# Kernel optimization log

Hardware: AMD Instinct MI355X
Metric: run time of the kernel (lower is better)

## Reference

```python
import jax, jax.numpy as jnp
import numpy as np

B, H, S, DK = 4, 12, 2048, 64

def setup_inputs() -> dict:
    key = jax.random.key(0)
    kq, kk, kv = jax.random.split(key, 3)
    Q = jax.random.normal(kq, (B, H, S, DK), dtype=jnp.float32)
    K = jax.random.normal(kk, (B, H, S, DK), dtype=jnp.float32)
    V = jax.random.normal(kv, (B, H, S, DK), dtype=jnp.float32)
    return {"Q": Q, "K": K, "V": V, "d_k": DK}

def reference(Q, K, V, d_k):
    scale = 1.0 / jnp.sqrt(jnp.float32(d_k))
    # scores: [B, H, S, S]
    scores = jnp.einsum('bhqd,bhkd->bhqk', Q, K) * scale
    attn = jax.nn.softmax(scores, axis=-1)
    context = jnp.einsum('bhqk,bhkd->bhqd', attn, V)
    return (context, attn)
```

## Files before the change

### kernel.cpp

```cpp
#include <hip/hip_runtime.h>


#define S_LEN 2048
#define D_K   64
#define NBH   48
#define VT_STRIDE 2080
#define CH    128
#define NCHUNK (S_LEN / CH)

typedef __attribute__((ext_vector_type(8))) short short8v;
typedef __attribute__((ext_vector_type(4))) short short4v;
typedef __attribute__((ext_vector_type(4))) float float4v;

__device__ inline unsigned short f2bf(float f) {
    union { float f; unsigned u; } c; c.f = f;
    unsigned u = c.u;
    return (unsigned short)((u + 0x7FFFu + ((u >> 16) & 1u)) >> 16);
}
__device__ inline float bf2f(unsigned short h) {
    union { unsigned u; float f; } c; c.u = ((unsigned)h) << 16; return c.f;
}

__device__ inline void wg_sync_lds() {
    asm volatile("s_waitcnt lgkmcnt(0)" ::: "memory");
    __builtin_amdgcn_s_barrier();
    __builtin_amdgcn_sched_barrier(0);
}

#define CEXP 0.18033688011112042f

__global__ __launch_bounds__(256)
void conv_k_kernel(const float* __restrict__ K, unsigned short* __restrict__ Kbf) {
    const size_t N = (size_t)NBH * S_LEN * D_K;
    for (size_t i = ((size_t)blockIdx.x * 256 + threadIdx.x) * 4; i < N;
         i += (size_t)gridDim.x * 256 * 4) {
        float4v v = *reinterpret_cast<const float4v*>(K + i);
        unsigned p0 = (unsigned)f2bf(v[0]) | ((unsigned)f2bf(v[1]) << 16);
        unsigned p1 = (unsigned)f2bf(v[2]) | ((unsigned)f2bf(v[3]) << 16);
        uint2 pk; pk.x = p0; pk.y = p1;
        *reinterpret_cast<uint2*>(Kbf + i) = pk;
    }
}

__global__ __launch_bounds__(256)
void trans_v_kernel(const float* __restrict__ V, unsigned short* __restrict__ VT) {
    const int bh = blockIdx.y;
    const int k0 = blockIdx.x * 64;
    __shared__ unsigned short tile[64][66];
    const int t = threadIdx.x;
    {
        const int kr = t >> 2, dq = t & 3;
        const float* src = V + (size_t)bh * S_LEN * D_K + (size_t)(k0 + kr) * D_K + dq * 16;
        #pragma unroll
        for (int i = 0; i < 4; ++i) {
            float4v v = *reinterpret_cast<const float4v*>(src + i * 4);
            #pragma unroll
            for (int j = 0; j < 4; ++j) tile[kr][dq * 16 + i * 4 + j] = f2bf(v[j]);
        }
    }
    __syncthreads();
    {
        const int d = t >> 2, kq = t & 3;
        unsigned pk[8];
        #pragma unroll
        for (int i = 0; i < 8; ++i) {
            unsigned lo = tile[kq * 16 + 2 * i][d];
            unsigned hi = tile[kq * 16 + 2 * i + 1][d];
            pk[i] = lo | (hi << 16);
        }
        unsigned* dst = reinterpret_cast<unsigned*>(
            VT + (size_t)bh * D_K * VT_STRIDE + (size_t)d * VT_STRIDE + k0 + kq * 16);
        uint4 a; a.x = pk[0]; a.y = pk[1]; a.z = pk[2]; a.w = pk[3];
        uint4 b; b.x = pk[4]; b.y = pk[5]; b.z = pk[6]; b.w = pk[7];
        reinterpret_cast<uint4*>(dst)[0] = a;
        reinterpret_cast<uint4*>(dst)[1] = b;
    }
}

__global__ __launch_bounds__(512, 6)
void sdpa_fused_kernel(const float* __restrict__ Qp,
                       const unsigned short* __restrict__ Kbf,
                       const unsigned short* __restrict__ VT,
                       float* __restrict__ ctx, float* __restrict__ attn) {
    const int qt   = blockIdx.x;
    const int bh   = blockIdx.y;
    const int tid  = threadIdx.x;
    const int w    = tid >> 6;
    const int lane = tid & 63;
    const int lq   = lane & 15;
    const int lg   = lane >> 4;
    const int qg   = qt * 128 + w * 16;
    const size_t base = (size_t)bh * S_LEN * D_K;

    __shared__ __align__(16) unsigned short kbuf[128 * 64];
    __shared__ __align__(16) unsigned short vbuf[64 * 128];
    __shared__ __align__(16) unsigned short pbw[8][16][40];

    short8v q0, q1;
    {
        const float* qr = Qp + base + (size_t)(qg + lq) * D_K + lg * 8;
        float4v qa = *reinterpret_cast<const float4v*>(qr);
        float4v qb = *reinterpret_cast<const float4v*>(qr + 4);
        float4v qc = *reinterpret_cast<const float4v*>(qr + 32);
        float4v qd = *reinterpret_cast<const float4v*>(qr + 36);
        #pragma unroll
        for (int j = 0; j < 4; ++j) {
            q0[j]     = (short)f2bf(qa[j]);
            q0[4 + j] = (short)f2bf(qb[j]);
            q1[j]     = (short)f2bf(qc[j]);
            q1[4 + j] = (short)f2bf(qd[j]);
        }
    }

    const int krow  = tid >> 2;
    const int kby0  = (tid & 3) * 16;
    const int kbi0  = krow * 64 + (((kby0)      ^ ((krow & 7) << 4)) >> 1);
    const int kbi1  = krow * 64 + (((kby0 + 64) ^ ((krow & 7) << 4)) >> 1);
    const unsigned short* ksrcb = Kbf + base + (size_t)krow * D_K + (kby0 >> 1);

    const int vrow  = tid >> 3;
    const int vby0  = (tid & 7) * 16;
    const int vbi0  = vrow * 128 + (((vby0)       ^ ((vrow & 15) << 4)) >> 1);
    const int vbi1  = vrow * 128 + (((vby0 + 128) ^ ((vrow & 15) << 4)) >> 1);
    const unsigned short* vsrcb = VT + (size_t)bh * D_K * VT_STRIDE
                                     + (size_t)vrow * VT_STRIDE + (vby0 >> 1);

    const int kswz = (lq & 7) << 4;
    const int koff0 = ((lg * 16)      ^ kswz) >> 1;
    const int koff1 = ((64 + lg * 16) ^ kswz) >> 1;
    const int vswz = lq << 4;

    float s = 0.f;
    for (int c = 0; c < NCHUNK; ++c) {
        short8v kr0 = *reinterpret_cast<const short8v*>(ksrcb + (size_t)c * CH * D_K);
        short8v kr1 = *reinterpret_cast<const short8v*>(ksrcb + (size_t)c * CH * D_K + 32);
        wg_sync_lds();
        *reinterpret_cast<short8v*>(&kbuf[kbi0]) = kr0;
        *reinterpret_cast<short8v*>(&kbuf[kbi1]) = kr1;
        wg_sync_lds();
        #pragma unroll
        for (int kt = 0; kt < 8; ++kt) {
            const int kl = kt * 16 + lq;
            short8v k0 = *reinterpret_cast<const short8v*>(&kbuf[kl * 64 + koff0]);
            short8v k1 = *reinterpret_cast<const short8v*>(&kbuf[kl * 64 + koff1]);
            float4v a = (float4v)0.0f;
            a = __builtin_amdgcn_mfma_f32_16x16x32_bf16(k0, q0, a, 0, 0, 0);
            a = __builtin_amdgcn_mfma_f32_16x16x32_bf16(k1, q1, a, 0, 0, 0);
            s += exp2f(a[0] * CEXP) + exp2f(a[1] * CEXP)
               + exp2f(a[2] * CEXP) + exp2f(a[3] * CEXP);
        }
    }
    s += __shfl_xor(s, 16, 64);
    s += __shfl_xor(s, 32, 64);
    const float rs_a = 1.0f / s;

    float4v cacc[4];
    #pragma unroll
    for (int dt = 0; dt < 4; ++dt) cacc[dt] = (float4v)0.0f;

    float* attnb = attn + (size_t)bh * S_LEN * S_LEN;

    for (int c = 0; c < NCHUNK; ++c) {
        short8v kr0 = *reinterpret_cast<const short8v*>(ksrcb + (size_t)c * CH * D_K);
        short8v kr1 = *reinterpret_cast<const short8v*>(ksrcb + (size_t)c * CH * D_K + 32);
        short8v vr0 = *reinterpret_cast<const short8v*>(vsrcb + c * CH);
        short8v vr1 = *reinterpret_cast<const short8v*>(vsrcb + c * CH + 64);
        wg_sync_lds();
        *reinterpret_cast<short8v*>(&kbuf[kbi0]) = kr0;
        *reinterpret_cast<short8v*>(&kbuf[kbi1]) = kr1;
        *reinterpret_cast<short8v*>(&vbuf[vbi0]) = vr0;
        *reinterpret_cast<short8v*>(&vbuf[vbi1]) = vr1;
        wg_sync_lds();

        #pragma unroll
        for (int s2 = 0; s2 < 4; ++s2) {
            #pragma unroll
            for (int t = 0; t < 2; ++t) {
                const int kt = s2 * 2 + t;
                const int kl = kt * 16 + lq;
                short8v k0 = *reinterpret_cast<const short8v*>(&kbuf[kl * 64 + koff0]);
                short8v k1 = *reinterpret_cast<const short8v*>(&kbuf[kl * 64 + koff1]);
                float4v a = (float4v)0.0f;
                a = __builtin_amdgcn_mfma_f32_16x16x32_bf16(k0, q0, a, 0, 0, 0);
                a = __builtin_amdgcn_mfma_f32_16x16x32_bf16(k1, q1, a, 0, 0, 0);
                float p0 = exp2f(a[0] * CEXP) * rs_a;
                float p1 = exp2f(a[1] * CEXP) * rs_a;
                float p2 = exp2f(a[2] * CEXP) * rs_a;
                float p3 = exp2f(a[3] * CEXP) * rs_a;
                uint2 pkv;
                pkv.x = (unsigned)f2bf(p0) | ((unsigned)f2bf(p1) << 16);
                pkv.y = (unsigned)f2bf(p2) | ((unsigned)f2bf(p3) << 16);
                *reinterpret_cast<uint2*>(&pbw[w][lq][t * 16 + lg * 4]) = pkv;
            }
            #pragma unroll
            for (int r2 = 0; r2 < 2; ++r2) {
                const int row = r2 * 8 + (lane >> 3);
                short4v p4 = *reinterpret_cast<const short4v*>(&pbw[w][row][(lane & 7) * 4]);
                float4v o;
                o[0] = bf2f((unsigned short)p4[0]);
                o[1] = bf2f((unsigned short)p4[1]);
                o[2] = bf2f((unsigned short)p4[2]);
                o[3] = bf2f((unsigned short)p4[3]);
                *reinterpret_cast<float4v*>(
                    &attnb[(size_t)(qg + row) * S_LEN + c * CH + s2 * 32 + (lane & 7) * 4]) = o;
            }
            short8v pa = *reinterpret_cast<const short8v*>(&pbw[w][lq][lg * 8]);
            #pragma unroll
            for (int dt = 0; dt < 4; ++dt) {
                const int d = dt * 16 + lq;
                short8v bv = *reinterpret_cast<const short8v*>(
                    &vbuf[d * 128 + (((s2 * 64 + lg * 16) ^ vswz) >> 1)]);
                cacc[dt] = __builtin_amdgcn_mfma_f32_16x16x32_bf16(pa, bv, cacc[dt], 0, 0, 0);
            }
        }
    }

    float* ctxb = ctx + base;
    #pragma unroll
    for (int dt = 0; dt < 4; ++dt)
        #pragma unroll
        for (int r = 0; r < 4; ++r)
            ctxb[(size_t)(qg + lg * 4 + r) * D_K + dt * 16 + lq] = cacc[dt][r];
}

__global__ __launch_bounds__(512)
void sdpa_fallback_kernel(const float* __restrict__ Qp, const float* __restrict__ Kp,
                          const float* __restrict__ Vp,
                          float* __restrict__ ctx, float* __restrict__ attn) {
    const int qt = blockIdx.x, bh = blockIdx.y, tid = threadIdx.x;
    const int w = tid >> 6, lane = tid & 63, lq = lane & 15, lg = lane >> 4;
    const int qg = qt * 16, kw = w * 256;
    const size_t base = (size_t)bh * S_LEN * D_K;
    __shared__ __align__(16) char smem_raw[8 * 16 * 136 * 2];
    __shared__ float red_s[16][8];
    auto pbuf = reinterpret_cast<unsigned short(*)[16][136]>(smem_raw);
    auto ctxp = reinterpret_cast<float(*)[16][64]>(smem_raw);

    short8v q0, q1;
    {
        const float* qr = Qp + base + (size_t)(qg + lq) * D_K + lg * 8;
        #pragma unroll
        for (int j = 0; j < 8; ++j) { q0[j] = (short)f2bf(qr[j]); q1[j] = (short)f2bf(qr[32 + j]); }
    }
    float4v acc[16];
    #pragma unroll
    for (int kt = 0; kt < 16; ++kt) acc[kt] = (float4v)0.0f;
    #pragma unroll
    for (int kt = 0; kt < 16; ++kt) {
        const float* kr = Kp + base + (size_t)(kw + kt * 16 + lq) * D_K + lg * 8;
        short8v k0, k1;
        #pragma unroll
        for (int j = 0; j < 8; ++j) { k0[j] = (short)f2bf(kr[j]); k1[j] = (short)f2bf(kr[32 + j]); }
        acc[kt] = __builtin_amdgcn_mfma_f32_16x16x32_bf16(k0, q0, acc[kt], 0, 0, 0);
        acc[kt] = __builtin_amdgcn_mfma_f32_16x16x32_bf16(k1, q1, acc[kt], 0, 0, 0);
    }
    float s = 0.f;
    #pragma unroll
    for (int kt = 0; kt < 16; ++kt)
        #pragma unroll
        for (int r = 0; r < 4; ++r) {
            float p = exp2f(acc[kt][r] * CEXP);
            acc[kt][r] = p; s += p;
        }
    s += __shfl_xor(s, 16, 64);
    s += __shfl_xor(s, 32, 64);
    if (lane < 16) red_s[lane][w] = s;
    __syncthreads();
    float gs = red_s[lq][0];
    #pragma unroll
    for (int ww = 1; ww < 8; ++ww) gs += red_s[lq][ww];
    const float rsv = 1.0f / gs;
    #pragma unroll
    for (int kt = 0; kt < 16; ++kt) acc[kt] = acc[kt] * rsv;

    float4v cacc[4];
    #pragma unroll
    for (int dt = 0; dt < 4; ++dt) cacc[dt] = (float4v)0.0f;
    #pragma unroll
    for (int half = 0; half < 2; ++half) {
        #pragma unroll
        for (int kth = 0; kth < 8; ++kth) {
            const int kt = half * 8 + kth;
            unsigned p01 = (unsigned)f2bf(acc[kt][0]) | ((unsigned)f2bf(acc[kt][1]) << 16);
            unsigned p23 = (unsigned)f2bf(acc[kt][2]) | ((unsigned)f2bf(acc[kt][3]) << 16);
            unsigned* dst = reinterpret_cast<unsigned*>(&pbuf[w][lq][kth * 16 + lg * 4]);
            dst[0] = p01; dst[1] = p23;
        }
        #pragma unroll
        for (int s2 = 0; s2 < 4; ++s2) {
            short8v pa = *reinterpret_cast<const short8v*>(&pbuf[w][lq][s2 * 32 + lg * 8]);
            const int kk = kw + half * 128 + s2 * 32 + lg * 8;
            #pragma unroll
            for (int dt = 0; dt < 4; ++dt) {
                short8v bv;
                #pragma unroll
                for (int j = 0; j < 8; ++j)
                    bv[j] = (short)f2bf(Vp[base + (size_t)(kk + j) * D_K + dt * 16 + lq]);
                cacc[dt] = __builtin_amdgcn_mfma_f32_16x16x32_bf16(pa, bv, cacc[dt], 0, 0, 0);
            }
        }
    }
    __syncthreads();
    #pragma unroll
    for (int dt = 0; dt < 4; ++dt)
        #pragma unroll
        for (int r = 0; r < 4; ++r)
            ctxp[w][lg * 4 + r][dt * 16 + lq] = cacc[dt][r];
    __syncthreads();
    float* ctxb = ctx + base;
    for (int idx = tid; idx < 16 * 64; idx += 512) {
        const int q = idx >> 6, d = idx & 63;
        float sum = 0.f;
        #pragma unroll
        for (int ww = 0; ww < 8; ++ww) sum += ctxp[ww][q][d];
        ctxb[(size_t)(qg + q) * D_K + d] = sum;
    }
    float* attnb = attn + (size_t)bh * S_LEN * S_LEN + (size_t)(qg + lq) * S_LEN + kw + lg * 4;
    #pragma unroll
    for (int kt = 0; kt < 16; ++kt)
        *reinterpret_cast<float4v*>(attnb + kt * 16) = acc[kt];
}

extern "C" void kernel_launch(void* const* d_in, const int* in_sizes, int n_in,
                              void* d_out, int out_size, void* d_ws, size_t ws_size,
                              hipStream_t stream) {
    const float* Q = (const float*)d_in[0];
    const float* K = (const float*)d_in[1];
    const float* V = (const float*)d_in[2];
    float* ctx  = (float*)d_out;
    float* attn = ctx + (size_t)NBH * S_LEN * D_K;

    const size_t nel  = (size_t)NBH * S_LEN * D_K;
    const size_t nvt  = (size_t)NBH * D_K * VT_STRIDE;
    const size_t need = (nel + nvt) * 2;

    if (ws_size >= need) {
        unsigned short* Kbf = (unsigned short*)d_ws;
        unsigned short* VT  = Kbf + nel;
        conv_k_kernel<<<2048, 256, 0, stream>>>(K, Kbf);
        trans_v_kernel<<<dim3(32, 48), 256, 0, stream>>>(V, VT);
        sdpa_fused_kernel<<<dim3(16, 48), 512, 0, stream>>>(Q, Kbf, VT, ctx, attn);
    } else {
        sdpa_fallback_kernel<<<dim3(128, 48), 512, 0, stream>>>(Q, K, V, ctx, attn);
    }
}
```

Baseline: 282.8 us.

## Prefetch next K/V chunk into registers, remap blocks per XCD, widen stats-pass chunks

Both passes now load the next chunk's K (and V) from global memory into registers right after the LDS barrier, so the global-load latency overlaps the MFMA and exp work on the current chunk. The first (row-sum) pass uses 256-row chunks in a merged LDS buffer, which halves its barrier count. Blocks are also remapped so that all query tiles of a given batch-head land on the same XCD, improving L2 reuse of K/V. The cost is higher register pressure from the prefetch buffers, which could lower occupancy under the 6-waves launch bound.

```diff
diff --git a/kernel.cpp b/kernel.cpp
--- a/kernel.cpp
+++ b/kernel.cpp
@@ -7,6 +7,8 @@
 #define VT_STRIDE 2080
 #define CH    128
 #define NCHUNK (S_LEN / CH)
+#define CH1   256
+#define NCH1  (S_LEN / CH1)
 
 typedef __attribute__((ext_vector_type(8))) short short8v;
 typedef __attribute__((ext_vector_type(4))) short short4v;
@@ -82,8 +84,12 @@
                        const unsigned short* __restrict__ Kbf,
                        const unsigned short* __restrict__ VT,
                        float* __restrict__ ctx, float* __restrict__ attn) {
-    const int qt   = blockIdx.x;
-    const int bh   = blockIdx.y;
+    const int f   = blockIdx.x + (blockIdx.y << 4);
+    const int xcd = f & 7;
+    const int j   = f >> 3;
+    const int bh  = xcd * 6 + (j >> 4);
+    const int qt  = j & 15;
+
     const int tid  = threadIdx.x;
     const int w    = tid >> 6;
     const int lane = tid & 63;
@@ -92,9 +98,9 @@
     const int qg   = qt * 128 + w * 16;
     const size_t base = (size_t)bh * S_LEN * D_K;
 
-    __shared__ __align__(16) unsigned short kbuf[128 * 64];
-    __shared__ __align__(16) unsigned short vbuf[64 * 128];
+    __shared__ __align__(16) unsigned short sbuf[256 * 64];
     __shared__ __align__(16) unsigned short pbw[8][16][40];
+    unsigned short* vbuf = sbuf + 128 * 64;
 
     short8v q0, q1;
     {
@@ -104,123 +110,147 @@
         float4v qc = *reinterpret_cast<const float4v*>(qr + 32);
         float4v qd = *reinterpret_cast<const float4v*>(qr + 36);
         #pragma unroll
-        for (int j = 0; j < 4; ++j) {
-            q0[j]     = (short)f2bf(qa[j]);
-            q0[4 + j] = (short)f2bf(qb[j]);
-            q1[j]     = (short)f2bf(qc[j]);
-            q1[4 + j] = (short)f2bf(qd[j]);
-        }
-    }
-
-    const int krow  = tid >> 2;
-    const int kby0  = (tid & 3) * 16;
-    const int kbi0  = krow * 64 + (((kby0)      ^ ((krow & 7) << 4)) >> 1);
-    const int kbi1  = krow * 64 + (((kby0 + 64) ^ ((krow & 7) << 4)) >> 1);
-    const unsigned short* ksrcb = Kbf + base + (size_t)krow * D_K + (kby0 >> 1);
-
-    const int vrow  = tid >> 3;
-    const int vby0  = (tid & 7) * 16;
-    const int vbi0  = vrow * 128 + (((vby0)       ^ ((vrow & 15) << 4)) >> 1);
-    const int vbi1  = vrow * 128 + (((vby0 + 128) ^ ((vrow & 15) << 4)) >> 1);
-    const unsigned short* vsrcb = VT + (size_t)bh * D_K * VT_STRIDE
-                                     + (size_t)vrow * VT_STRIDE + (vby0 >> 1);
-
-    const int kswz = (lq & 7) << 4;
+        for (int jj = 0; jj < 4; ++jj) {
+            q0[jj]     = (short)f2bf(qa[jj]);
+            q0[4 + jj] = (short)f2bf(qb[jj]);
+            q1[jj]     = (short)f2bf(qc[jj]);
+            q1[4 + jj] = (short)f2bf(qd[jj]);
+        }
+    }
+
+    const int kswz  = (lq & 7) << 4;
     const int koff0 = ((lg * 16)      ^ kswz) >> 1;
     const int koff1 = ((64 + lg * 16) ^ kswz) >> 1;
-    const int vswz = lq << 4;
-
-    float s = 0.f;
-    for (int c = 0; c < NCHUNK; ++c) {
-        short8v kr0 = *reinterpret_cast<const short8v*>(ksrcb + (size_t)c * CH * D_K);
-        short8v kr1 = *reinterpret_cast<const short8v*>(ksrcb + (size_t)c * CH * D_K + 32);
-        wg_sync_lds();
-        *reinterpret_cast<short8v*>(&kbuf[kbi0]) = kr0;
-        *reinterpret_cast<short8v*>(&kbuf[kbi1]) = kr1;
-        wg_sync_lds();
-        #pragma unroll
-        for (int kt = 0; kt < 8; ++kt) {
-            const int kl = kt * 16 + lq;
-            short8v k0 = *reinterpret_cast<const short8v*>(&kbuf[kl * 64 + koff0]);
-            short8v k1 = *reinterpret_cast<const short8v*>(&kbuf[kl * 64 + koff1]);
-            float4v a = (float4v)0.0f;
-            a = __builtin_amdgcn_mfma_f32_16x16x32_bf16(k0, q0, a, 0, 0, 0);
-            a = __builtin_amdgcn_mfma_f32_16x16x32_bf16(k1, q1, a, 0, 0, 0);
-            s += exp2f(a[0] * CEXP) + exp2f(a[1] * CEXP)
-               + exp2f(a[2] * CEXP) + exp2f(a[3] * CEXP);
-        }
-    }
-    s += __shfl_xor(s, 16, 64);
-    s += __shfl_xor(s, 32, 64);
-    const float rs_a = 1.0f / s;
-
-    float4v cacc[4];
-    #pragma unroll
-    for (int dt = 0; dt < 4; ++dt) cacc[dt] = (float4v)0.0f;
-
-    float* attnb = attn + (size_t)bh * S_LEN * S_LEN;
-
-    for (int c = 0; c < NCHUNK; ++c) {
-        short8v kr0 = *reinterpret_cast<const short8v*>(ksrcb + (size_t)c * CH * D_K);
-        short8v kr1 = *reinterpret_cast<const short8v*>(ksrcb + (size_t)c * CH * D_K + 32);
-        short8v vr0 = *reinterpret_cast<const short8v*>(vsrcb + c * CH);
-        short8v vr1 = *reinterpret_cast<const short8v*>(vsrcb + c * CH + 64);
-        wg_sync_lds();
-        *reinterpret_cast<short8v*>(&kbuf[kbi0]) = kr0;
-        *reinterpret_cast<short8v*>(&kbuf[kbi1]) = kr1;
-        *reinterpret_cast<short8v*>(&vbuf[vbi0]) = vr0;
-        *reinterpret_cast<short8v*>(&vbuf[vbi1]) = vr1;
-        wg_sync_lds();
-
-        #pragma unroll
-        for (int s2 = 0; s2 < 4; ++s2) {
-            #pragma unroll
-            for (int t = 0; t < 2; ++t) {
-                const int kt = s2 * 2 + t;
+    const int vswz  = lq << 4;
+
+    {
+        const int row0 = tid >> 3;
+        const int by   = (tid & 7) * 16;
+        const int sidx0 = row0 * 64 + ((by ^ ((row0 & 7) << 4)) >> 1);
+        const unsigned short* ksrc1 = Kbf + base + (size_t)row0 * D_K + (by >> 1);
+
+        short8v ka[4], kan[4];
+        #pragma unroll
+        for (int r = 0; r < 4; ++r)
+            ka[r] = *reinterpret_cast<const short8v*>(ksrc1 + (size_t)r * 64 * D_K);
+
+        float s = 0.f;
+        for (int c = 0; c < NCH1; ++c) {
+            wg_sync_lds();
+            #pragma unroll
+            for (int r = 0; r < 4; ++r)
+                *reinterpret_cast<short8v*>(&sbuf[sidx0 + r * 4096]) = ka[r];
+            wg_sync_lds();
+            const int cn = (c + 1 < NCH1) ? c + 1 : c;
+            #pragma unroll
+            for (int r = 0; r < 4; ++r)
+                kan[r] = *reinterpret_cast<const short8v*>(
+                    ksrc1 + (size_t)(cn * CH1 + r * 64) * D_K);
+            #pragma unroll
+            for (int kt = 0; kt < 16; ++kt) {
                 const int kl = kt * 16 + lq;
-                short8v k0 = *reinterpret_cast<const short8v*>(&kbuf[kl * 64 + koff0]);
-                short8v k1 = *reinterpret_cast<const short8v*>(&kbuf[kl * 64 + koff1]);
+                short8v k0 = *reinterpret_cast<const short8v*>(&sbuf[kl * 64 + koff0]);
+                short8v k1 = *reinterpret_cast<const short8v*>(&sbuf[kl * 64 + koff1]);
                 float4v a = (float4v)0.0f;
                 a = __builtin_amdgcn_mfma_f32_16x16x32_bf16(k0, q0, a, 0, 0, 0);
                 a = __builtin_amdgcn_mfma_f32_16x16x32_bf16(k1, q1, a, 0, 0, 0);
-                float p0 = exp2f(a[0] * CEXP) * rs_a;
-                float p1 = exp2f(a[1] * CEXP) * rs_a;
-                float p2 = exp2f(a[2] * CEXP) * rs_a;
-                float p3 = exp2f(a[3] * CEXP) * rs_a;
-                uint2 pkv;
-                pkv.x = (unsigned)f2bf(p0) | ((unsigned)f2bf(p1) << 16);
-                pkv.y = (unsigned)f2bf(p2) | ((unsigned)f2bf(p3) << 16);
-                *reinterpret_cast<uint2*>(&pbw[w][lq][t * 16 + lg * 4]) = pkv;
+                s += exp2f(a[0] * CEXP) + exp2f(a[1] * CEXP)
+                   + exp2f(a[2] * CEXP) + exp2f(a[3] * CEXP);
             }
             #pragma unroll
-            for (int r2 = 0; r2 < 2; ++r2) {
-                const int row = r2 * 8 + (lane >> 3);
-                short4v p4 = *reinterpret_cast<const short4v*>(&pbw[w][row][(lane & 7) * 4]);
-                float4v o;
-                o[0] = bf2f((unsigned short)p4[0]);
-                o[1] = bf2f((unsigned short)p4[1]);
-                o[2] = bf2f((unsigned short)p4[2]);
-                o[3] = bf2f((unsigned short)p4[3]);
-                *reinterpret_cast<float4v*>(
-                    &attnb[(size_t)(qg + row) * S_LEN + c * CH + s2 * 32 + (lane & 7) * 4]) = o;
+            for (int r = 0; r < 4; ++r) ka[r] = kan[r];
+        }
+        s += __shfl_xor(s, 16, 64);
+        s += __shfl_xor(s, 32, 64);
+        float rs_a = 1.0f / s;
+
+        const int krow = tid >> 2;
+        const int kby0 = (tid & 3) * 16;
+        const int kbi0 = krow * 64 + (((kby0)      ^ ((krow & 7) << 4)) >> 1);
+        const int kbi1 = krow * 64 + (((kby0 + 64) ^ ((krow & 7) << 4)) >> 1);
+        const unsigned short* ksrcb = Kbf + base + (size_t)krow * D_K + (kby0 >> 1);
+
+        const int vrow = tid >> 3;
+        const int vby0 = (tid & 7) * 16;
+        const int vbi0 = vrow * 128 + (((vby0)       ^ ((vrow & 15) << 4)) >> 1);
+        const int vbi1 = vrow * 128 + (((vby0 + 128) ^ ((vrow & 15) << 4)) >> 1);
+        const unsigned short* vsrcb = VT + (size_t)bh * D_K * VT_STRIDE
+                                         + (size_t)vrow * VT_STRIDE + (vby0 >> 1);
+
+        float4v cacc[4];
+        #pragma unroll
+        for (int dt = 0; dt < 4; ++dt) cacc[dt] = (float4v)0.0f;
+
+        float* attnb = attn + (size_t)bh * S_LEN * S_LEN;
+
+        short8v kr0 = *reinterpret_cast<const short8v*>(ksrcb);
+        short8v kr1 = *reinterpret_cast<const short8v*>(ksrcb + 32);
+        short8v vr0 = *reinterpret_cast<const short8v*>(vsrcb);
+        short8v vr1 = *reinterpret_cast<const short8v*>(vsrcb + 64);
+
+        for (int c = 0; c < NCHUNK; ++c) {
+            wg_sync_lds();
+            *reinterpret_cast<short8v*>(&sbuf[kbi0]) = kr0;
+            *reinterpret_cast<short8v*>(&sbuf[kbi1]) = kr1;
+            *reinterpret_cast<short8v*>(&vbuf[vbi0]) = vr0;
+            *reinterpret_cast<short8v*>(&vbuf[vbi1]) = vr1;
+            wg_sync_lds();
+            const int cn = (c + 1 < NCHUNK) ? c + 1 : c;
+            kr0 = *reinterpret_cast<const short8v*>(ksrcb + (size_t)cn * CH * D_K);
+            kr1 = *reinterpret_cast<const short8v*>(ksrcb + (size_t)cn * CH * D_K + 32);
+            vr0 = *reinterpret_cast<const short8v*>(vsrcb + cn * CH);
+            vr1 = *reinterpret_cast<const short8v*>(vsrcb + cn * CH + 64);
+
+            #pragma unroll
+            for (int s2 = 0; s2 < 4; ++s2) {
+                #pragma unroll
+                for (int t = 0; t < 2; ++t) {
+                    const int kt = s2 * 2 + t;
+                    const int kl = kt * 16 + lq;
+                    short8v k0 = *reinterpret_cast<const short8v*>(&sbuf[kl * 64 + koff0]);
+                    short8v k1 = *reinterpret_cast<const short8v*>(&sbuf[kl * 64 + koff1]);
+                    float4v a = (float4v)0.0f;
+                    a = __builtin_amdgcn_mfma_f32_16x16x32_bf16(k0, q0, a, 0, 0, 0);
+                    a = __builtin_amdgcn_mfma_f32_16x16x32_bf16(k1, q1, a, 0, 0, 0);
+                    float p0 = exp2f(a[0] * CEXP) * rs_a;
+                    float p1 = exp2f(a[1] * CEXP) * rs_a;
+                    float p2 = exp2f(a[2] * CEXP) * rs_a;
+                    float p3 = exp2f(a[3] * CEXP) * rs_a;
+                    uint2 pkv;
+                    pkv.x = (unsigned)f2bf(p0) | ((unsigned)f2bf(p1) << 16);
+                    pkv.y = (unsigned)f2bf(p2) | ((unsigned)f2bf(p3) << 16);
+                    *reinterpret_cast<uint2*>(&pbw[w][lq][t * 16 + lg * 4]) = pkv;
+                }
+                #pragma unroll
+                for (int r2 = 0; r2 < 2; ++r2) {
+                    const int row = r2 * 8 + (lane >> 3);
+                    short4v p4 = *reinterpret_cast<const short4v*>(&pbw[w][row][(lane & 7) * 4]);
+                    float4v o;
+                    o[0] = bf2f((unsigned short)p4[0]);
+                    o[1] = bf2f((unsigned short)p4[1]);
+                    o[2] = bf2f((unsigned short)p4[2]);
+                    o[3] = bf2f((unsigned short)p4[3]);
+                    *reinterpret_cast<float4v*>(
+                        &attnb[(size_t)(qg + row) * S_LEN + c * CH + s2 * 32 + (lane & 7) * 4]) = o;
+                }
+                short8v pa = *reinterpret_cast<const short8v*>(&pbw[w][lq][lg * 8]);
+                #pragma unroll
+                for (int dt = 0; dt < 4; ++dt) {
+                    const int d = dt * 16 + lq;
+                    short8v bv = *reinterpret_cast<const short8v*>(
+                        &vbuf[d * 128 + (((s2 * 64 + lg * 16) ^ vswz) >> 1)]);
+                    cacc[dt] = __builtin_amdgcn_mfma_f32_16x16x32_bf16(pa, bv, cacc[dt], 0, 0, 0);
+                }
             }
-            short8v pa = *reinterpret_cast<const short8v*>(&pbw[w][lq][lg * 8]);
-            #pragma unroll
-            for (int dt = 0; dt < 4; ++dt) {
-                const int d = dt * 16 + lq;
-                short8v bv = *reinterpret_cast<const short8v*>(
-                    &vbuf[d * 128 + (((s2 * 64 + lg * 16) ^ vswz) >> 1)]);
-                cacc[dt] = __builtin_amdgcn_mfma_f32_16x16x32_bf16(pa, bv, cacc[dt], 0, 0, 0);
-            }
-        }
-    }
-
-    float* ctxb = ctx + base;
-    #pragma unroll
-    for (int dt = 0; dt < 4; ++dt)
-        #pragma unroll
-        for (int r = 0; r < 4; ++r)
-            ctxb[(size_t)(qg + lg * 4 + r) * D_K + dt * 16 + lq] = cacc[dt][r];
+        }
+
+        float* ctxb = ctx + base;
+        #pragma unroll
+        for (int dt = 0; dt < 4; ++dt)
+            #pragma unroll
+            for (int r = 0; r < 4; ++r)
+                ctxb[(size_t)(qg + lg * 4 + r) * D_K + dt * 16 + lq] = cacc[dt][r];
+    }
 }
 
 __global__ __launch_bounds__(512)
```

Result: slower. 304.0 us (+7.5%).

## Double-buffer K/V LDS tiles with register prefetch in both softmax passes

Applied to the files above, without the earlier changes.

Replaces the single-buffered K and V LDS tiles with one ping-pong buffer and prefetches the next-next chunk into registers while computing on the current one. Each chunk now needs one barrier instead of two. The second pass uses 64-key chunks so K and V fit together in each half of the buffer, which doubles its iteration count and changes the V tile layout and swizzle. The aim is to hide global-load latency behind MFMA and exp work. The cost is more live registers and a different LDS access pattern.

```diff
diff --git a/kernel.cpp b/kernel.cpp
--- a/kernel.cpp
+++ b/kernel.cpp
@@ -5,8 +5,6 @@
 #define D_K   64
 #define NBH   48
 #define VT_STRIDE 2080
-#define CH    128
-#define NCHUNK (S_LEN / CH)
 
 typedef __attribute__((ext_vector_type(8))) short short8v;
 typedef __attribute__((ext_vector_type(4))) short short4v;
@@ -92,8 +90,7 @@
     const int qg   = qt * 128 + w * 16;
     const size_t base = (size_t)bh * S_LEN * D_K;
 
-    __shared__ __align__(16) unsigned short kbuf[128 * 64];
-    __shared__ __align__(16) unsigned short vbuf[64 * 128];
+    __shared__ __align__(16) unsigned short sbuf[2 * 128 * 64];
     __shared__ __align__(16) unsigned short pbw[8][16][40];
 
     short8v q0, q1;
@@ -104,123 +101,154 @@
         float4v qc = *reinterpret_cast<const float4v*>(qr + 32);
         float4v qd = *reinterpret_cast<const float4v*>(qr + 36);
         #pragma unroll
-        for (int j = 0; j < 4; ++j) {
-            q0[j]     = (short)f2bf(qa[j]);
-            q0[4 + j] = (short)f2bf(qb[j]);
-            q1[j]     = (short)f2bf(qc[j]);
-            q1[4 + j] = (short)f2bf(qd[j]);
-        }
-    }
-
-    const int krow  = tid >> 2;
-    const int kby0  = (tid & 3) * 16;
-    const int kbi0  = krow * 64 + (((kby0)      ^ ((krow & 7) << 4)) >> 1);
-    const int kbi1  = krow * 64 + (((kby0 + 64) ^ ((krow & 7) << 4)) >> 1);
-    const unsigned short* ksrcb = Kbf + base + (size_t)krow * D_K + (kby0 >> 1);
-
-    const int vrow  = tid >> 3;
-    const int vby0  = (tid & 7) * 16;
-    const int vbi0  = vrow * 128 + (((vby0)       ^ ((vrow & 15) << 4)) >> 1);
-    const int vbi1  = vrow * 128 + (((vby0 + 128) ^ ((vrow & 15) << 4)) >> 1);
-    const unsigned short* vsrcb = VT + (size_t)bh * D_K * VT_STRIDE
-                                     + (size_t)vrow * VT_STRIDE + (vby0 >> 1);
-
-    const int kswz = (lq & 7) << 4;
+        for (int jj = 0; jj < 4; ++jj) {
+            q0[jj]     = (short)f2bf(qa[jj]);
+            q0[4 + jj] = (short)f2bf(qb[jj]);
+            q1[jj]     = (short)f2bf(qc[jj]);
+            q1[4 + jj] = (short)f2bf(qd[jj]);
+        }
+    }
+
+    const int kswz  = (lq & 7) << 4;
     const int koff0 = ((lg * 16)      ^ kswz) >> 1;
     const int koff1 = ((64 + lg * 16) ^ kswz) >> 1;
-    const int vswz = lq << 4;
-
-    float s = 0.f;
-    for (int c = 0; c < NCHUNK; ++c) {
-        short8v kr0 = *reinterpret_cast<const short8v*>(ksrcb + (size_t)c * CH * D_K);
-        short8v kr1 = *reinterpret_cast<const short8v*>(ksrcb + (size_t)c * CH * D_K + 32);
+
+    float rs_a;
+    {
+        const int s1row = tid >> 2;
+        const int s1by  = (tid & 3) * 32;
+        const int s1i0  = s1row * 64 + (((s1by)      ^ ((s1row & 7) << 4)) >> 1);
+        const int s1i1  = s1row * 64 + (((s1by + 16) ^ ((s1row & 7) << 4)) >> 1);
+        const unsigned short* s1src = Kbf + base + (size_t)s1row * D_K + (s1by >> 1);
+
+        short8v ra, rb;
+        ra = *reinterpret_cast<const short8v*>(s1src);
+        rb = *reinterpret_cast<const short8v*>(s1src + 8);
+        *reinterpret_cast<short8v*>(&sbuf[s1i0]) = ra;
+        *reinterpret_cast<short8v*>(&sbuf[s1i1]) = rb;
+        ra = *reinterpret_cast<const short8v*>(s1src + (size_t)128 * 64);
+        rb = *reinterpret_cast<const short8v*>(s1src + (size_t)128 * 64 + 8);
         wg_sync_lds();
-        *reinterpret_cast<short8v*>(&kbuf[kbi0]) = kr0;
-        *reinterpret_cast<short8v*>(&kbuf[kbi1]) = kr1;
-        wg_sync_lds();
-        #pragma unroll
-        for (int kt = 0; kt < 8; ++kt) {
-            const int kl = kt * 16 + lq;
-            short8v k0 = *reinterpret_cast<const short8v*>(&kbuf[kl * 64 + koff0]);
-            short8v k1 = *reinterpret_cast<const short8v*>(&kbuf[kl * 64 + koff1]);
-            float4v a = (float4v)0.0f;
-            a = __builtin_amdgcn_mfma_f32_16x16x32_bf16(k0, q0, a, 0, 0, 0);
-            a = __builtin_amdgcn_mfma_f32_16x16x32_bf16(k1, q1, a, 0, 0, 0);
-            s += exp2f(a[0] * CEXP) + exp2f(a[1] * CEXP)
-               + exp2f(a[2] * CEXP) + exp2f(a[3] * CEXP);
-        }
-    }
-    s += __shfl_xor(s, 16, 64);
-    s += __shfl_xor(s, 32, 64);
-    const float rs_a = 1.0f / s;
-
-    float4v cacc[4];
-    #pragma unroll
-    for (int dt = 0; dt < 4; ++dt) cacc[dt] = (float4v)0.0f;
-
-    float* attnb = attn + (size_t)bh * S_LEN * S_LEN;
-
-    for (int c = 0; c < NCHUNK; ++c) {
-        short8v kr0 = *reinterpret_cast<const short8v*>(ksrcb + (size_t)c * CH * D_K);
-        short8v kr1 = *reinterpret_cast<const short8v*>(ksrcb + (size_t)c * CH * D_K + 32);
-        short8v vr0 = *reinterpret_cast<const short8v*>(vsrcb + c * CH);
-        short8v vr1 = *reinterpret_cast<const short8v*>(vsrcb + c * CH + 64);
-        wg_sync_lds();
-        *reinterpret_cast<short8v*>(&kbuf[kbi0]) = kr0;
-        *reinterpret_cast<short8v*>(&kbuf[kbi1]) = kr1;
-        *reinterpret_cast<short8v*>(&vbuf[vbi0]) = vr0;
-        *reinterpret_cast<short8v*>(&vbuf[vbi1]) = vr1;
-        wg_sync_lds();
-
-        #pragma unroll
-        for (int s2 = 0; s2 < 4; ++s2) {
-            #pragma unroll
-            for (int t = 0; t < 2; ++t) {
-                const int kt = s2 * 2 + t;
+
+        float s = 0.f;
+        int cur = 0;
+        for (int c = 0; c < 16; ++c) {
+            if (c < 15) {
+                const int o = (cur ^ 1) * 8192;
+                *reinterpret_cast<short8v*>(&sbuf[o + s1i0]) = ra;
+                *reinterpret_cast<short8v*>(&sbuf[o + s1i1]) = rb;
+            }
+            if (c < 14) {
+                ra = *reinterpret_cast<const short8v*>(s1src + (size_t)(c + 2) * 128 * 64);
+                rb = *reinterpret_cast<const short8v*>(s1src + (size_t)(c + 2) * 128 * 64 + 8);
+            }
+            const int cb = cur * 8192;
+            #pragma unroll
+            for (int kt = 0; kt < 8; ++kt) {
                 const int kl = kt * 16 + lq;
-                short8v k0 = *reinterpret_cast<const short8v*>(&kbuf[kl * 64 + koff0]);
-                short8v k1 = *reinterpret_cast<const short8v*>(&kbuf[kl * 64 + koff1]);
+                short8v k0 = *reinterpret_cast<const short8v*>(&sbuf[cb + kl * 64 + koff0]);
+                short8v k1 = *reinterpret_cast<const short8v*>(&sbuf[cb + kl * 64 + koff1]);
                 float4v a = (float4v)0.0f;
                 a = __builtin_amdgcn_mfma_f32_16x16x32_bf16(k0, q0, a, 0, 0, 0);
                 a = __builtin_amdgcn_mfma_f32_16x16x32_bf16(k1, q1, a, 0, 0, 0);
-                float p0 = exp2f(a[0] * CEXP) * rs_a;
-                float p1 = exp2f(a[1] * CEXP) * rs_a;
-                float p2 = exp2f(a[2] * CEXP) * rs_a;
-                float p3 = exp2f(a[3] * CEXP) * rs_a;
-                uint2 pkv;
-                pkv.x = (unsigned)f2bf(p0) | ((unsigned)f2bf(p1) << 16);
-                pkv.y = (unsigned)f2bf(p2) | ((unsigned)f2bf(p3) << 16);
-                *reinterpret_cast<uint2*>(&pbw[w][lq][t * 16 + lg * 4]) = pkv;
-            }
-            #pragma unroll
-            for (int r2 = 0; r2 < 2; ++r2) {
-                const int row = r2 * 8 + (lane >> 3);
-                short4v p4 = *reinterpret_cast<const short4v*>(&pbw[w][row][(lane & 7) * 4]);
-                float4v o;
-                o[0] = bf2f((unsigned short)p4[0]);
-                o[1] = bf2f((unsigned short)p4[1]);
-                o[2] = bf2f((unsigned short)p4[2]);
-                o[3] = bf2f((unsigned short)p4[3]);
-                *reinterpret_cast<float4v*>(
-                    &attnb[(size_t)(qg + row) * S_LEN + c * CH + s2 * 32 + (lane & 7) * 4]) = o;
-            }
-            short8v pa = *reinterpret_cast<const short8v*>(&pbw[w][lq][lg * 8]);
-            #pragma unroll
-            for (int dt = 0; dt < 4; ++dt) {
-                const int d = dt * 16 + lq;
-                short8v bv = *reinterpret_cast<const short8v*>(
-                    &vbuf[d * 128 + (((s2 * 64 + lg * 16) ^ vswz) >> 1)]);
-                cacc[dt] = __builtin_amdgcn_mfma_f32_16x16x32_bf16(pa, bv, cacc[dt], 0, 0, 0);
-            }
-        }
-    }
-
-    float* ctxb = ctx + base;
-    #pragma unroll
-    for (int dt = 0; dt < 4; ++dt)
-        #pragma unroll
-        for (int r = 0; r < 4; ++r)
-            ctxb[(size_t)(qg + lg * 4 + r) * D_K + dt * 16 + lq] = cacc[dt][r];
+                s += exp2f(a[0] * CEXP) + exp2f(a[1] * CEXP)
+                   + exp2f(a[2] * CEXP) + exp2f(a[3] * CEXP);
+            }
+            wg_sync_lds();
+            cur ^= 1;
+        }
+        s += __shfl_xor(s, 16, 64);
+        s += __shfl_xor(s, 32, 64);
+        rs_a = 1.0f / s;
+    }
+
+    {
+        const int krow = tid >> 3;
+        const int kby  = (tid & 7) * 16;
+        const int kbi  = krow * 64 + ((kby ^ ((krow & 7) << 4)) >> 1);
+        const int vbi  = 4096 + krow * 64 + ((kby ^ ((krow & 7) << 4)) >> 1);
+        const unsigned short* ksrc = Kbf + base + (size_t)krow * D_K + (kby >> 1);
+        const unsigned short* vsrc = VT + (size_t)bh * D_K * VT_STRIDE
+                                        + (size_t)krow * VT_STRIDE + (kby >> 1);
+
+        float4v cacc[4];
+        #pragma unroll
+        for (int dt = 0; dt < 4; ++dt) cacc[dt] = (float4v)0.0f;
+        float* attnb = attn + (size_t)bh * S_LEN * S_LEN;
+
+        short8v kreg, vreg;
+        kreg = *reinterpret_cast<const short8v*>(ksrc);
+        vreg = *reinterpret_cast<const short8v*>(vsrc);
+        *reinterpret_cast<short8v*>(&sbuf[kbi]) = kreg;
+        *reinterpret_cast<short8v*>(&sbuf[vbi]) = vreg;
+        kreg = *reinterpret_cast<const short8v*>(ksrc + (size_t)64 * D_K);
+        vreg = *reinterpret_cast<const short8v*>(vsrc + 64);
+        wg_sync_lds();
+
+        int cur = 0;
+        for (int c = 0; c < 32; ++c) {
+            if (c < 31) {
+                const int o = (cur ^ 1) * 8192;
+                *reinterpret_cast<short8v*>(&sbuf[o + kbi]) = kreg;
+                *reinterpret_cast<short8v*>(&sbuf[o + vbi]) = vreg;
+            }
+            if (c < 30) {
+                kreg = *reinterpret_cast<const short8v*>(ksrc + (size_t)(c + 2) * 64 * D_K);
+                vreg = *reinterpret_cast<const short8v*>(vsrc + (c + 2) * 64);
+            }
+            const int cb = cur * 8192;
+            #pragma unroll
+            for (int s2 = 0; s2 < 2; ++s2) {
+                #pragma unroll
+                for (int t = 0; t < 2; ++t) {
+                    const int kt = s2 * 2 + t;
+                    const int kl = kt * 16 + lq;
+                    short8v k0 = *reinterpret_cast<const short8v*>(&sbuf[cb + kl * 64 + koff0]);
+                    short8v k1 = *reinterpret_cast<const short8v*>(&sbuf[cb + kl * 64 + koff1]);
+                    float4v a = (float4v)0.0f;
+                    a = __builtin_amdgcn_mfma_f32_16x16x32_bf16(k0, q0, a, 0, 0, 0);
+                    a = __builtin_amdgcn_mfma_f32_16x16x32_bf16(k1, q1, a, 0, 0, 0);
+                    float p0 = exp2f(a[0] * CEXP) * rs_a;
+                    float p1 = exp2f(a[1] * CEXP) * rs_a;
+                    float p2 = exp2f(a[2] * CEXP) * rs_a;
+                    float p3 = exp2f(a[3] * CEXP) * rs_a;
+                    uint2 pkv;
+                    pkv.x = (unsigned)f2bf(p0) | ((unsigned)f2bf(p1) << 16);
+                    pkv.y = (unsigned)f2bf(p2) | ((unsigned)f2bf(p3) << 16);
+                    *reinterpret_cast<uint2*>(&pbw[w][lq][t * 16 + lg * 4]) = pkv;
+                }
+                #pragma unroll
+                for (int r2 = 0; r2 < 2; ++r2) {
+                    const int row = r2 * 8 + (lane >> 3);
+                    short4v p4 = *reinterpret_cast<const short4v*>(&pbw[w][row][(lane & 7) * 4]);
+                    float4v o;
+                    o[0] = bf2f((unsigned short)p4[0]);
+                    o[1] = bf2f((unsigned short)p4[1]);
+                    o[2] = bf2f((unsigned short)p4[2]);
+                    o[3] = bf2f((unsigned short)p4[3]);
+                    *reinterpret_cast<float4v*>(
+                        &attnb[(size_t)(qg + row) * S_LEN + c * 64 + s2 * 32 + (lane & 7) * 4]) = o;
+                }
+                short8v pa = *reinterpret_cast<const short8v*>(&pbw[w][lq][lg * 8]);
+                #pragma unroll
+                for (int dt = 0; dt < 4; ++dt) {
+                    const int d = dt * 16 + lq;
+                    short8v bv = *reinterpret_cast<const short8v*>(
+                        &sbuf[cb + 4096 + d * 64 + (((s2 * 64 + lg * 16) ^ ((d & 7) << 4)) >> 1)]);
+                    cacc[dt] = __builtin_amdgcn_mfma_f32_16x16x32_bf16(pa, bv, cacc[dt], 0, 0, 0);
+                }
+            }
+            wg_sync_lds();
+            cur ^= 1;
+        }
+
+        float* ctxb = ctx + base;
+        #pragma unroll
+        for (int dt = 0; dt < 4; ++dt)
+            #pragma unroll
+            for (int r = 0; r < 4; ++r)
+                ctxb[(size_t)(qg + lg * 4 + r) * D_K + dt * 16 + lq] = cacc[dt][r];
+    }
 }
 
 __global__ __launch_bounds__(512)
```

New measurement: 301.8 us. 1.07x slower.

## Process 32 query rows per wave with 256-thread blocks to reuse K/V fragments

Applied to the files above, without the earlier changes.

Each wave now handles two 16-row query tiles instead of one, so every K and V fragment read from LDS feeds two MFMAs. The block shrinks from 512 to 256 threads while the grid stays the same, and each thread stages twice as much K/V into LDS. This is meant to cut LDS read traffic and barrier overhead per unit of work. The cost is more registers (two accumulator sets, four Q fragments), lower occupancy, and fewer waves available to hide latency.

```diff
diff --git a/kernel.cpp b/kernel.cpp
--- a/kernel.cpp
+++ b/kernel.cpp
@@ -77,7 +77,7 @@
     }
 }
 
-__global__ __launch_bounds__(512, 6)
+__global__ __launch_bounds__(256, 3)
 void sdpa_fused_kernel(const float* __restrict__ Qp,
                        const unsigned short* __restrict__ Kbf,
                        const unsigned short* __restrict__ VT,
@@ -89,39 +89,54 @@
     const int lane = tid & 63;
     const int lq   = lane & 15;
     const int lg   = lane >> 4;
-    const int qg   = qt * 128 + w * 16;
+    const int qg0  = qt * 128 + w * 32;
     const size_t base = (size_t)bh * S_LEN * D_K;
 
     __shared__ __align__(16) unsigned short kbuf[128 * 64];
     __shared__ __align__(16) unsigned short vbuf[64 * 128];
-    __shared__ __align__(16) unsigned short pbw[8][16][40];
-
-    short8v q0, q1;
+    __shared__ __align__(16) unsigned short pbw[4][32][40];
+
+    short8v qa0, qa1, qb0, qb1;
     {
-        const float* qr = Qp + base + (size_t)(qg + lq) * D_K + lg * 8;
-        float4v qa = *reinterpret_cast<const float4v*>(qr);
-        float4v qb = *reinterpret_cast<const float4v*>(qr + 4);
-        float4v qc = *reinterpret_cast<const float4v*>(qr + 32);
-        float4v qd = *reinterpret_cast<const float4v*>(qr + 36);
+        const float* qrA = Qp + base + (size_t)(qg0 + lq) * D_K + lg * 8;
+        const float* qrB = qrA + (size_t)16 * D_K;
+        float4v a0 = *reinterpret_cast<const float4v*>(qrA);
+        float4v a1 = *reinterpret_cast<const float4v*>(qrA + 4);
+        float4v a2 = *reinterpret_cast<const float4v*>(qrA + 32);
+        float4v a3 = *reinterpret_cast<const float4v*>(qrA + 36);
+        float4v b0 = *reinterpret_cast<const float4v*>(qrB);
+        float4v b1 = *reinterpret_cast<const float4v*>(qrB + 4);
+        float4v b2 = *reinterpret_cast<const float4v*>(qrB + 32);
+        float4v b3 = *reinterpret_cast<const float4v*>(qrB + 36);
         #pragma unroll
         for (int j = 0; j < 4; ++j) {
-            q0[j]     = (short)f2bf(qa[j]);
-            q0[4 + j] = (short)f2bf(qb[j]);
-            q1[j]     = (short)f2bf(qc[j]);
-            q1[4 + j] = (short)f2bf(qd[j]);
+            qa0[j]     = (short)f2bf(a0[j]);
+            qa0[4 + j] = (short)f2bf(a1[j]);
+            qa1[j]     = (short)f2bf(a2[j]);
+            qa1[4 + j] = (short)f2bf(a3[j]);
+            qb0[j]     = (short)f2bf(b0[j]);
+            qb0[4 + j] = (short)f2bf(b1[j]);
+            qb1[j]     = (short)f2bf(b2[j]);
+            qb1[4 + j] = (short)f2bf(b3[j]);
         }
     }
 
     const int krow  = tid >> 2;
     const int kby0  = (tid & 3) * 16;
-    const int kbi0  = krow * 64 + (((kby0)      ^ ((krow & 7) << 4)) >> 1);
-    const int kbi1  = krow * 64 + (((kby0 + 64) ^ ((krow & 7) << 4)) >> 1);
+    const int ksw   = (krow & 7) << 4;
+    const int kbiA0 = krow * 64 + (((kby0)      ^ ksw) >> 1);
+    const int kbiA1 = krow * 64 + (((kby0 + 64) ^ ksw) >> 1);
+    const int kbiB0 = (krow + 64) * 64 + (((kby0)      ^ ksw) >> 1);
+    const int kbiB1 = (krow + 64) * 64 + (((kby0 + 64) ^ ksw) >> 1);
     const unsigned short* ksrcb = Kbf + base + (size_t)krow * D_K + (kby0 >> 1);
 
-    const int vrow  = tid >> 3;
-    const int vby0  = (tid & 7) * 16;
-    const int vbi0  = vrow * 128 + (((vby0)       ^ ((vrow & 15) << 4)) >> 1);
-    const int vbi1  = vrow * 128 + (((vby0 + 128) ^ ((vrow & 15) << 4)) >> 1);
+    const int vrow  = tid >> 2;
+    const int vsw   = (vrow & 15) << 4;
+    const int vby0  = (tid & 3) * 16;
+    int vbi[4];
+    #pragma unroll
+    for (int j = 0; j < 4; ++j)
+        vbi[j] = vrow * 128 + (((vby0 + j * 64) ^ vsw) >> 1);
     const unsigned short* vsrcb = VT + (size_t)bh * D_K * VT_STRIDE
                                      + (size_t)vrow * VT_STRIDE + (vby0 >> 1);
 
@@ -130,46 +145,68 @@
     const int koff1 = ((64 + lg * 16) ^ kswz) >> 1;
     const int vswz = lq << 4;
 
-    float s = 0.f;
+    float sA0 = 0.f, sA1 = 0.f, sB0 = 0.f, sB1 = 0.f;
     for (int c = 0; c < NCHUNK; ++c) {
-        short8v kr0 = *reinterpret_cast<const short8v*>(ksrcb + (size_t)c * CH * D_K);
-        short8v kr1 = *reinterpret_cast<const short8v*>(ksrcb + (size_t)c * CH * D_K + 32);
+        const unsigned short* kc = ksrcb + (size_t)c * CH * D_K;
+        short8v r0 = *reinterpret_cast<const short8v*>(kc);
+        short8v r1 = *reinterpret_cast<const short8v*>(kc + 32);
+        short8v r2 = *reinterpret_cast<const short8v*>(kc + (size_t)64 * D_K);
+        short8v r3 = *reinterpret_cast<const short8v*>(kc + (size_t)64 * D_K + 32);
         wg_sync_lds();
-        *reinterpret_cast<short8v*>(&kbuf[kbi0]) = kr0;
-        *reinterpret_cast<short8v*>(&kbuf[kbi1]) = kr1;
+        *reinterpret_cast<short8v*>(&kbuf[kbiA0]) = r0;
+        *reinterpret_cast<short8v*>(&kbuf[kbiA1]) = r1;
+        *reinterpret_cast<short8v*>(&kbuf[kbiB0]) = r2;
+        *reinterpret_cast<short8v*>(&kbuf[kbiB1]) = r3;
         wg_sync_lds();
         #pragma unroll
         for (int kt = 0; kt < 8; ++kt) {
             const int kl = kt * 16 + lq;
             short8v k0 = *reinterpret_cast<const short8v*>(&kbuf[kl * 64 + koff0]);
             short8v k1 = *reinterpret_cast<const short8v*>(&kbuf[kl * 64 + koff1]);
-            float4v a = (float4v)0.0f;
-            a = __builtin_amdgcn_mfma_f32_16x16x32_bf16(k0, q0, a, 0, 0, 0);
-            a = __builtin_amdgcn_mfma_f32_16x16x32_bf16(k1, q1, a, 0, 0, 0);
-            s += exp2f(a[0] * CEXP) + exp2f(a[1] * CEXP)
-               + exp2f(a[2] * CEXP) + exp2f(a[3] * CEXP);
-        }
-    }
-    s += __shfl_xor(s, 16, 64);
-    s += __shfl_xor(s, 32, 64);
-    const float rs_a = 1.0f / s;
-
-    float4v cacc[4];
-    #pragma unroll
-    for (int dt = 0; dt < 4; ++dt) cacc[dt] = (float4v)0.0f;
+            float4v aA = (float4v)0.0f, aB = (float4v)0.0f;
+            aA = __builtin_amdgcn_mfma_f32_16x16x32_bf16(k0, qa0, aA, 0, 0, 0);
+            aA = __builtin_amdgcn_mfma_f32_16x16x32_bf16(k1, qa1, aA, 0, 0, 0);
+            aB = __builtin_amdgcn_mfma_f32_16x16x32_bf16(k0, qb0, aB, 0, 0, 0);
+            aB = __builtin_amdgcn_mfma_f32_16x16x32_bf16(k1, qb1, aB, 0, 0, 0);
+            sA0 += exp2f(aA[0] * CEXP) + exp2f(aA[1] * CEXP);
+            sA1 += exp2f(aA[2] * CEXP) + exp2f(aA[3] * CEXP);
+            sB0 += exp2f(aB[0] * CEXP) + exp2f(aB[1] * CEXP);
+            sB1 += exp2f(aB[2] * CEXP) + exp2f(aB[3] * CEXP);
+        }
+    }
+    float sA = sA0 + sA1, sB = sB0 + sB1;
+    sA += __shfl_xor(sA, 16, 64);
+    sA += __shfl_xor(sA, 32, 64);
+    sB += __shfl_xor(sB, 16, 64);
+    sB += __shfl_xor(sB, 32, 64);
+    const float rsA = 1.0f / sA;
+    const float rsB = 1.0f / sB;
+
+    float4v caccA[4], caccB[4];
+    #pragma unroll
+    for (int dt = 0; dt < 4; ++dt) { caccA[dt] = (float4v)0.0f; caccB[dt] = (float4v)0.0f; }
 
     float* attnb = attn + (size_t)bh * S_LEN * S_LEN;
 
     for (int c = 0; c < NCHUNK; ++c) {
-        short8v kr0 = *reinterpret_cast<const short8v*>(ksrcb + (size_t)c * CH * D_K);
-        short8v kr1 = *reinterpret_cast<const short8v*>(ksrcb + (size_t)c * CH * D_K + 32);
-        short8v vr0 = *reinterpret_cast<const short8v*>(vsrcb + c * CH);
-        short8v vr1 = *reinterpret_cast<const short8v*>(vsrcb + c * CH + 64);
+        const unsigned short* kc = ksrcb + (size_t)c * CH * D_K;
+        short8v r0 = *reinterpret_cast<const short8v*>(kc);
+        short8v r1 = *reinterpret_cast<const short8v*>(kc + 32);
+        short8v r2 = *reinterpret_cast<const short8v*>(kc + (size_t)64 * D_K);
+        short8v r3 = *reinterpret_cast<const short8v*>(kc + (size_t)64 * D_K + 32);
+        short8v v0 = *reinterpret_cast<const short8v*>(vsrcb + c * CH);
+        short8v v1 = *reinterpret_cast<const short8v*>(vsrcb + c * CH + 32);
+        short8v v2 = *reinterpret_cast<const short8v*>(vsrcb + c * CH + 64);
+        short8v v3 = *reinterpret_cast<const short8v*>(vsrcb + c * CH + 96);
         wg_sync_lds();
-        *reinterpret_cast<short8v*>(&kbuf[kbi0]) = kr0;
-        *reinterpret_cast<short8v*>(&kbuf[kbi1]) = kr1;
-        *reinterpret_cast<short8v*>(&vbuf[vbi0]) = vr0;
-        *reinterpret_cast<short8v*>(&vbuf[vbi1]) = vr1;
+        *reinterpret_cast<short8v*>(&kbuf[kbiA0]) = r0;
+        *reinterpret_cast<short8v*>(&kbuf[kbiA1]) = r1;
+        *reinterpret_cast<short8v*>(&kbuf[kbiB0]) = r2;
+        *reinterpret_cast<short8v*>(&kbuf[kbiB1]) = r3;
+        *reinterpret_cast<short8v*>(&vbuf[vbi[0]]) = v0;
+        *reinterpret_cast<short8v*>(&vbuf[vbi[1]]) = v1;
+        *reinterpret_cast<short8v*>(&vbuf[vbi[2]]) = v2;
+        *reinterpret_cast<short8v*>(&vbuf[vbi[3]]) = v3;
         wg_sync_lds();
 
         #pragma unroll
@@ -180,20 +217,25 @@
                 const int kl = kt * 16 + lq;
                 short8v k0 = *reinterpret_cast<const short8v*>(&kbuf[kl * 64 + koff0]);
                 short8v k1 = *reinterpret_cast<const short8v*>(&kbuf[kl * 64 + koff1]);
-                float4v a = (float4v)0.0f;
-                a = __builtin_amdgcn_mfma_f32_16x16x32_bf16(k0, q0, a, 0, 0, 0);
-                a = __builtin_amdgcn_mfma_f32_16x16x32_bf16(k1, q1, a, 0, 0, 0);
-                float p0 = exp2f(a[0] * CEXP) * rs_a;
-                float p1 = exp2f(a[1] * CEXP) * rs_a;
-                float p2 = exp2f(a[2] * CEXP) * rs_a;
-                float p3 = exp2f(a[3] * CEXP) * rs_a;
-                uint2 pkv;
-                pkv.x = (unsigned)f2bf(p0) | ((unsigned)f2bf(p1) << 16);
-                pkv.y = (unsigned)f2bf(p2) | ((unsigned)f2bf(p3) << 16);
-                *reinterpret_cast<uint2*>(&pbw[w][lq][t * 16 + lg * 4]) = pkv;
+                float4v aA = (float4v)0.0f, aB = (float4v)0.0f;
+                aA = __builtin_amdgcn_mfma_f32_16x16x32_bf16(k0, qa0, aA, 0, 0, 0);
+                aA = __builtin_amdgcn_mfma_f32_16x16x32_bf16(k1, qa1, aA, 0, 0, 0);
+                aB = __builtin_amdgcn_mfma_f32_16x16x32_bf16(k0, qb0, aB, 0, 0, 0);
+                aB = __builtin_amdgcn_mfma_f32_16x16x32_bf16(k1, qb1, aB, 0, 0, 0);
+                uint2 pA, pB;
+                pA.x = (unsigned)f2bf(exp2f(aA[0] * CEXP) * rsA)
+                     | ((unsigned)f2bf(exp2f(aA[1] * CEXP) * rsA) << 16);
+                pA.y = (unsigned)f2bf(exp2f(aA[2] * CEXP) * rsA)
+                     | ((unsigned)f2bf(exp2f(aA[3] * CEXP) * rsA) << 16);
+                pB.x = (unsigned)f2bf(exp2f(aB[0] * CEXP) * rsB)
+                     | ((unsigned)f2bf(exp2f(aB[1] * CEXP) * rsB) << 16);
+                pB.y = (unsigned)f2bf(exp2f(aB[2] * CEXP) * rsB)
+                     | ((unsigned)f2bf(exp2f(aB[3] * CEXP) * rsB) << 16);
+                *reinterpret_cast<uint2*>(&pbw[w][lq][t * 16 + lg * 4]) = pA;
+                *reinterpret_cast<uint2*>(&pbw[w][16 + lq][t * 16 + lg * 4]) = pB;
             }
             #pragma unroll
-            for (int r2 = 0; r2 < 2; ++r2) {
+            for (int r2 = 0; r2 < 4; ++r2) {
                 const int row = r2 * 8 + (lane >> 3);
                 short4v p4 = *reinterpret_cast<const short4v*>(&pbw[w][row][(lane & 7) * 4]);
                 float4v o;
@@ -202,15 +244,17 @@
                 o[2] = bf2f((unsigned short)p4[2]);
                 o[3] = bf2f((unsigned short)p4[3]);
                 *reinterpret_cast<float4v*>(
-                    &attnb[(size_t)(qg + row) * S_LEN + c * CH + s2 * 32 + (lane & 7) * 4]) = o;
+                    &attnb[(size_t)(qg0 + row) * S_LEN + c * CH + s2 * 32 + (lane & 7) * 4]) = o;
             }
-            short8v pa = *reinterpret_cast<const short8v*>(&pbw[w][lq][lg * 8]);
+            short8v paA = *reinterpret_cast<const short8v*>(&pbw[w][lq][lg * 8]);
+            short8v paB = *reinterpret_cast<const short8v*>(&pbw[w][16 + lq][lg * 8]);
             #pragma unroll
             for (int dt = 0; dt < 4; ++dt) {
                 const int d = dt * 16 + lq;
                 short8v bv = *reinterpret_cast<const short8v*>(
                     &vbuf[d * 128 + (((s2 * 64 + lg * 16) ^ vswz) >> 1)]);
-                cacc[dt] = __builtin_amdgcn_mfma_f32_16x16x32_bf16(pa, bv, cacc[dt], 0, 0, 0);
+                caccA[dt] = __builtin_amdgcn_mfma_f32_16x16x32_bf16(paA, bv, caccA[dt], 0, 0, 0);
+                caccB[dt] = __builtin_amdgcn_mfma_f32_16x16x32_bf16(paB, bv, caccB[dt], 0, 0, 0);
             }
         }
     }
@@ -219,8 +263,10 @@
     #pragma unroll
     for (int dt = 0; dt < 4; ++dt)
         #pragma unroll
-        for (int r = 0; r < 4; ++r)
-            ctxb[(size_t)(qg + lg * 4 + r) * D_K + dt * 16 + lq] = cacc[dt][r];
+        for (int r = 0; r < 4; ++r) {
+            ctxb[(size_t)(qg0 + lg * 4 + r) * D_K + dt * 16 + lq] = caccA[dt][r];
+            ctxb[(size_t)(qg0 + 16 + lg * 4 + r) * D_K + dt * 16 + lq] = caccB[dt][r];
+        }
 }
 
 __global__ __launch_bounds__(512)
@@ -339,7 +385,7 @@
         unsigned short* VT  = Kbf + nel;
         conv_k_kernel<<<2048, 256, 0, stream>>>(K, Kbf);
         trans_v_kernel<<<dim3(32, 48), 256, 0, stream>>>(V, VT);
-        sdpa_fused_kernel<<<dim3(16, 48), 512, 0, stream>>>(Q, Kbf, VT, ctx, attn);
+        sdpa_fused_kernel<<<dim3(16, 48), 256, 0, stream>>>(Q, Kbf, VT, ctx, attn);
     } else {
         sdpa_fallback_kernel<<<dim3(128, 48), 512, 0, stream>>>(Q, K, V, ctx, attn);
     }
```

After: 262.2 us (median of 2 runs). 7.3% less time.
